# Kernel optimization log

Hardware: AMD Instinct MI355X
Metric: run time of the kernel (lower is better)

## Reference

```python
import jax, jax.numpy as jnp
import numpy as np
from jax import lax

C = 64
KD = 16  # in_channels // k_factor
KS = 3
DN = ('NCHW', 'OIHW', 'NCHW')


def setup_inputs() -> dict:
    key = jax.random.key(0)
    ks = jax.random.split(key, 9)
    B, H, W = 4, 128, 128
    s = 0.05
    return {
        'x': jax.random.normal(ks[0], (B, C, H, W), jnp.float32),
        'y': jax.random.normal(ks[1], (B, C, H, W), jnp.float32),
        'z': jax.random.normal(ks[2], (B, C, H, W), jnp.float32),
        'Wq': jax.random.normal(ks[3], (C, 1, KS, KS), jnp.float32) * s,   # depthwise
        'bq': jax.random.normal(ks[4], (C,), jnp.float32) * s,
        'Wk': jax.random.normal(ks[5], (KD, C, KS, KS), jnp.float32) * s,
        'bk': jax.random.normal(ks[6], (KD,), jnp.float32) * s,
        'wv': jax.random.normal(ks[7], (KD,), jnp.float32) * s,           # 1x1 conv 1->KD
        'bv': jax.random.normal(ks[8], (KD,), jnp.float32) * s,
    }


def reference(x, y, z, Wq, bq, Wk, bk, wv, bv):
    # Q: depthwise 3x3 conv + ReLU on y -> [B,C,H,W]
    q = jax.nn.relu(
        lax.conv_general_dilated(y, Wq, (1, 1), 'SAME',
                                 dimension_numbers=DN, feature_group_count=C)
        + bq[None, :, None, None])
    # K: 3x3 conv C->KD + ReLU on x -> [B,KD,H,W], shared across the C channel axis
    k = jax.nn.relu(
        lax.conv_general_dilated(x, Wk, (1, 1), 'SAME', dimension_numbers=DN)
        + bk[None, :, None, None])
    # V: 1x1 conv 1->KD + ReLU applied per input channel of z -> [B,C,KD,H,W]
    v = jax.nn.relu(z[:, :, None] * wv[None, None, :, None, None]
                    + bv[None, None, :, None, None])
    # Degenerate SDPA: head_dim=1 so scale=1; softmax over the KD 'sequence' axis.
    scores = q[:, :, None] * k[:, None]              # [B,C,KD,H,W]
    attn = jax.nn.softmax(scores, axis=2)
    return jnp.sum(attn * v, axis=2)                 # [B,C,H,W]
```

## Files before the change

### kernel.cpp

```cpp
#include <hip/hip_runtime.h>

#define HH 128
#define WW 128
#define CC 64
#define KD 16
#define HW (HH * WW)
#define HWB (HW * 4)
#define TOTBYTES (4u * CC * HW * 4u)
#define OOB_SENT 0x40000000

typedef __attribute__((ext_vector_type(4))) int   int32x4_t;
typedef __attribute__((ext_vector_type(4))) float floatx4;
typedef __attribute__((ext_vector_type(2))) float floatx2;

__device__ floatx4 llvm_amdgcn_raw_buffer_load_v4f32(int32x4_t srsrc, int voffset,
                                                     int soffset, int aux)
    __asm("llvm.amdgcn.raw.buffer.load.v4f32");
__device__ floatx2 llvm_amdgcn_raw_buffer_load_v2f32(int32x4_t srsrc, int voffset,
                                                     int soffset, int aux)
    __asm("llvm.amdgcn.raw.buffer.load.v2f32");

__device__ inline int32x4_t make_srd(const void* p, unsigned bytes) {
    const unsigned long long a = (unsigned long long)p;
    int32x4_t r;
    r.x = (int)(a & 0xffffffffull);
    r.y = (int)(a >> 32);
    r.z = (int)bytes;
    r.w = 0x00020000;
    return r;
}

#if __has_builtin(__builtin_amdgcn_exp2f)
#define FAST_EXP2(x) __builtin_amdgcn_exp2f(x)
#define KLOG2E 1.44269504088896340736f
#else
#define FAST_EXP2(x) __expf(x)
#define KLOG2E 1.0f
#endif

__global__ __launch_bounds__(512, 1) void repack_wk(const float* __restrict__ Wk,
                                                    float* __restrict__ wsr) {
    const int e = blockIdx.x * 512 + threadIdx.x;
    const int d = e & 15;
    const int r = e >> 4;
    const int t = r % 9;
    const int c = r / 9;
    wsr[e] = Wk[(d * CC + c) * 9 + t];
}

__global__ __launch_bounds__(512, 4) void gatev_fused(
    const float* __restrict__ x, const float* __restrict__ y,
    const float* __restrict__ z,
    const float* __restrict__ wsr,
    const float* __restrict__ Wq, const float* __restrict__ bq,
    const float* __restrict__ bk,
    const float* __restrict__ wv, const float* __restrict__ bv,
    float* __restrict__ out)
{
    __shared__ float lds[16384];

    const int tid  = threadIdx.x;
    const int g    = __builtin_amdgcn_readfirstlane(tid >> 6);
    const int lane = tid & 63;
    const int px16 = lane & 15, py = lane >> 4;
    const int b    = blockIdx.z;
    const int w0   = blockIdx.x * 32 + px16 * 2;
    const int h    = blockIdx.y * 4 + py;
    const int pix  = h * WW + w0;
    const int p0   = py * 32 + px16 * 2;

    const int32x4_t rx = make_srd(x, TOTBYTES);
    const int32x4_t ry = make_srd(y, TOTBYTES);
    const int32x4_t rz = make_srd(z, TOTBYTES);

    const int colb = (w0 > 0 ? w0 - 1 : 0) * 4;
    int rowB[3];
#pragma unroll
    for (int r = 0; r < 3; ++r) {
        const int rr = h - 1 + r;
        rowB[r] = (rr >= 0 && rr < HH) ? rr * WW * 4 + colb : OOB_SENT;
    }
    const bool  intw = (blockIdx.x > 0) & (blockIdx.x < (WW / 32 - 1));
    const float mL = (w0 > 0) ? 1.f : 0.f;
    const float mR = (w0 + 2 < WW) ? 1.f : 0.f;
    const bool  w0e = (w0 == 0);

    const int base = b * CC * HWB;
    const int c0   = __builtin_amdgcn_readfirstlane(g * 8);

    auto mktaps = [&](const floatx4& f, float (&s)[4]) {
        if (intw) { s[0] = f.x; s[1] = f.y; s[2] = f.z; s[3] = f.w; }
        else {
            s[0] = f.x * mL;
            s[1] = w0e ? f.x : f.y;
            s[2] = w0e ? f.y : f.z;
            s[3] = (w0e ? f.z : f.w) * mR;
        }
    };

    floatx2 aP0[8], aP1[8];
#pragma unroll
    for (int i = 0; i < 8; ++i) { aP0[i] = (floatx2){0.f, 0.f}; aP1[i] = (floatx2){0.f, 0.f}; }

    auto load3 = [&](floatx4 (&f)[3], int so) {
#pragma unroll
        for (int r = 0; r < 3; ++r)
            f[r] = llvm_amdgcn_raw_buffer_load_v4f32(rx, rowB[r], so, 0);
    };
    auto compute = [&](const floatx4 (&f)[3], const float* wp) {
        float s[3][4];
#pragma unroll
        for (int r = 0; r < 3; ++r) mktaps(f[r], s[r]);
#pragma unroll
        for (int t = 0; t < 9; ++t) {
            const int tr = t / 3, tc = t % 3;
            const floatx2 t0 = {s[tr][tc],     s[tr][tc]};
            const floatx2 t1 = {s[tr][tc + 1], s[tr][tc + 1]};
#pragma unroll
            for (int j = 0; j < 4; ++j) {
                const floatx4 w4 = *(const floatx4*)&wp[t * 16 + j * 4];
                const floatx2 lo = __builtin_shufflevector(w4, w4, 0, 1);
                const floatx2 hi = __builtin_shufflevector(w4, w4, 2, 3);
                aP0[2 * j + 0] = __builtin_elementwise_fma(lo, t0, aP0[2 * j + 0]);
                aP0[2 * j + 1] = __builtin_elementwise_fma(hi, t0, aP0[2 * j + 1]);
                aP1[2 * j + 0] = __builtin_elementwise_fma(lo, t1, aP1[2 * j + 0]);
                aP1[2 * j + 1] = __builtin_elementwise_fma(hi, t1, aP1[2 * j + 1]);
            }
        }
    };

    {
        floatx4 f0[3], f1[3];
        load3(f0, base + c0 * HWB);
#pragma unroll
        for (int cp = 0; cp < 4; ++cp) {
            load3(f1, base + (c0 + 2 * cp + 1) * HWB);
            compute(f0, wsr + (c0 + 2 * cp) * 144);
            load3(f0, base + (c0 + 2 * cp + 2) * HWB);
            compute(f1, wsr + (c0 + 2 * cp + 1) * 144);
        }
    }

#pragma unroll
    for (int i = 0; i < 8; ++i) {
        *(floatx2*)&lds[g * 2048 + (2 * i + 0) * 128 + p0] = (floatx2){aP0[i].x, aP1[i].x};
        *(floatx2*)&lds[g * 2048 + (2 * i + 1) * 128 + p0] = (floatx2){aP0[i].y, aP1[i].y};
    }
    __syncthreads();

#pragma unroll
    for (int rep = 0; rep < 4; ++rep) {
        const int idx = tid + rep * 512;
        float s = lds[idx];
#pragma unroll
        for (int gg = 1; gg < 8; ++gg) s += lds[gg * 2048 + idx];
        const int d = idx >> 7;
        lds[idx] = fmaxf(s + bk[d], 0.f) * KLOG2E;
    }
    __syncthreads();

    floatx2 kl2[16];
#pragma unroll
    for (int d = 0; d < KD; ++d)
        kl2[d] = *(const floatx2*)&lds[d * 128 + p0];

    auto process = [&](const floatx4 (&f)[3], floatx2 z2, int c) {
        const float* wq = Wq + c * 9;
        float s[3][4];
#pragma unroll
        for (int r = 0; r < 3; ++r) mktaps(f[r], s[r]);
        floatx2 q2 = {bq[c], bq[c]};
#pragma unroll
        for (int t = 0; t < 9; ++t) {
            const int tr = t / 3, tc = t % 3;
            const floatx2 tp2 = {s[tr][tc], s[tr][tc + 1]};
            const floatx2 wq2 = {wq[t], wq[t]};
            q2 = __builtin_elementwise_fma(wq2, tp2, q2);
        }
        const floatx2 zero2 = {0.f, 0.f};
        q2 = __builtin_elementwise_max(q2, zero2);

        floatx2 num2 = zero2, den2 = zero2;
#pragma unroll
        for (int d = 0; d < KD; ++d) {
            const floatx2 s2 = q2 * kl2[d];
            floatx2 e2;
            e2.x = FAST_EXP2(s2.x);
            e2.y = FAST_EXP2(s2.y);
            const floatx2 wv2 = {wv[d], wv[d]};
            const floatx2 bv2 = {bv[d], bv[d]};
            const floatx2 v2 = __builtin_elementwise_max(
                __builtin_elementwise_fma(z2, wv2, bv2), zero2);
            num2 = __builtin_elementwise_fma(e2, v2, num2);
            den2 = den2 + e2;
        }
        floatx2 o2;
        o2.x = __fdividef(num2.x, den2.x);
        o2.y = __fdividef(num2.y, den2.y);
        *(floatx2*)&out[(size_t)b * CC * HW + (size_t)c * HW + pix] = o2;
    };

    auto load3y = [&](floatx4 (&f)[3], floatx2& zz, int so) {
#pragma unroll
        for (int r = 0; r < 3; ++r)
            f[r] = llvm_amdgcn_raw_buffer_load_v4f32(ry, rowB[r], so, 0);
        zz = llvm_amdgcn_raw_buffer_load_v2f32(rz, pix * 4, so, 0);
    };

    {
        floatx4 fy0[3], fy1[3];
        floatx2 z0, z1;
        load3y(fy0, z0, base + c0 * HWB);
#pragma unroll
        for (int cp = 0; cp < 4; ++cp) {
            load3y(fy1, z1, base + (c0 + 2 * cp + 1) * HWB);
            process(fy0, z0, c0 + 2 * cp);
            load3y(fy0, z0, base + (c0 + 2 * cp + 2) * HWB);
            process(fy1, z1, c0 + 2 * cp + 1);
        }
    }
}

extern "C" void kernel_launch(void* const* d_in, const int* in_sizes, int n_in,
                              void* d_out, int out_size, void* d_ws, size_t ws_size,
                              hipStream_t stream) {
    const float* x  = (const float*)d_in[0];
    const float* y  = (const float*)d_in[1];
    const float* z  = (const float*)d_in[2];
    const float* Wq = (const float*)d_in[3];
    const float* bq = (const float*)d_in[4];
    const float* Wk = (const float*)d_in[5];
    const float* bk = (const float*)d_in[6];
    const float* wv = (const float*)d_in[7];
    const float* bv = (const float*)d_in[8];
    float* out = (float*)d_out;
    float* wsr = (float*)d_ws;

    hipLaunchKernelGGL(repack_wk, dim3(18), dim3(512), 0, stream, Wk, wsr);

    dim3 grid(WW / 32, HH / 4, 4);
    dim3 block(512);
    hipLaunchKernelGGL(gatev_fused, grid, block, 0, stream,
                       x, y, z, wsr, Wq, bq, bk, wv, bv, out);
}
```

Baseline: 48.98 us.

## Split fused kernel into separate K-conv and attention kernels via workspace

Result: slower. 50.03 us (+2.2%).

```diff
diff --git a/kernel.cpp b/kernel.cpp
--- a/kernel.cpp
+++ b/kernel.cpp
@@ -46,6 +46,222 @@
     const int t = r % 9;
     const int c = r / 9;
     wsr[e] = Wk[(d * CC + c) * 9 + t];
+}
+
+__global__ __launch_bounds__(512, 8) void kconv(
+    const float* __restrict__ x, const float* __restrict__ wsr,
+    const float* __restrict__ bk, float* __restrict__ kout)
+{
+    __shared__ float lds[8 * KD * 64];
+
+    const int tid  = threadIdx.x;
+    const int g    = __builtin_amdgcn_readfirstlane(tid >> 6);
+    const int lane = tid & 63;
+    const int px   = lane & 15, py = lane >> 4;
+    const int b    = blockIdx.z;
+    const int h    = blockIdx.y * 4 + py;
+    const int w    = blockIdx.x * 16 + px;
+
+    const int32x4_t rx = make_srd(x, TOTBYTES);
+
+    const int colb = (w > 0 ? w - 1 : 0) * 4;
+    int rowB[3];
+#pragma unroll
+    for (int r = 0; r < 3; ++r) {
+        const int rr = h - 1 + r;
+        rowB[r] = (rr >= 0 && rr < HH) ? rr * WW * 4 + colb : OOB_SENT;
+    }
+    const float mL = (w > 0) ? 1.f : 0.f;
+    const float mR = (w < WW - 1) ? 1.f : 0.f;
+    const bool  w0e = (w == 0);
+
+    const int base = b * CC * HWB;
+    const int c0   = __builtin_amdgcn_readfirstlane(g * 8);
+
+    floatx2 a[8];
+#pragma unroll
+    for (int i = 0; i < 8; ++i) a[i] = (floatx2){0.f, 0.f};
+
+    auto load3 = [&](floatx4 (&f)[3], int so) {
+#pragma unroll
+        for (int r = 0; r < 3; ++r)
+            f[r] = llvm_amdgcn_raw_buffer_load_v4f32(rx, rowB[r], so, 0);
+    };
+    auto compute = [&](const floatx4 (&f)[3], const float* wp) {
+        float tp[9];
+#pragma unroll
+        for (int r = 0; r < 3; ++r) {
+            tp[r * 3 + 0] = f[r].x * mL;
+            tp[r * 3 + 1] = w0e ? f[r].x : f[r].y;
+            tp[r * 3 + 2] = (w0e ? f[r].y : f[r].z) * mR;
+        }
+#pragma unroll
+        for (int t = 0; t < 9; ++t) {
+            const floatx2 t2 = {tp[t], tp[t]};
+#pragma unroll
+            for (int j = 0; j < 4; ++j) {
+                const floatx4 w4 = *(const floatx4*)&wp[t * 16 + j * 4];
+                const floatx2 lo = __builtin_shufflevector(w4, w4, 0, 1);
+                const floatx2 hi = __builtin_shufflevector(w4, w4, 2, 3);
+                a[2 * j + 0] = __builtin_elementwise_fma(lo, t2, a[2 * j + 0]);
+                a[2 * j + 1] = __builtin_elementwise_fma(hi, t2, a[2 * j + 1]);
+            }
+        }
+    };
+
+    {
+        floatx4 f0[3], f1[3];
+        load3(f0, base + c0 * HWB);
+#pragma unroll
+        for (int cp = 0; cp < 4; ++cp) {
+            load3(f1, base + (c0 + 2 * cp + 1) * HWB);
+            compute(f0, wsr + (c0 + 2 * cp) * 144);
+            load3(f0, base + (c0 + 2 * cp + 2) * HWB);
+            compute(f1, wsr + (c0 + 2 * cp + 1) * 144);
+        }
+    }
+
+#pragma unroll
+    for (int i = 0; i < 8; ++i) {
+        lds[g * 1024 + (2 * i + 0) * 64 + lane] = a[i].x;
+        lds[g * 1024 + (2 * i + 1) * 64 + lane] = a[i].y;
+    }
+    __syncthreads();
+
+#pragma unroll
+    for (int rep = 0; rep < 2; ++rep) {
+        const int idx = tid + rep * 512;
+        float s = lds[idx];
+#pragma unroll
+        for (int gg = 1; gg < 8; ++gg) s += lds[gg * 1024 + idx];
+        const int d   = idx >> 6;
+        const int pxl = idx & 63;
+        const int hh  = blockIdx.y * 4 + (pxl >> 4);
+        const int ww  = blockIdx.x * 16 + (pxl & 15);
+        kout[(b * KD + d) * HW + hh * WW + ww] =
+            fmaxf(s + bk[d], 0.f) * KLOG2E;
+    }
+}
+
+__global__ __launch_bounds__(512, 4) void attn(
+    const float* __restrict__ y, const float* __restrict__ z,
+    const float* __restrict__ kout,
+    const float* __restrict__ Wq, const float* __restrict__ bq,
+    const float* __restrict__ wv, const float* __restrict__ bv,
+    float* __restrict__ out)
+{
+    __shared__ float klds[KD * 128];
+
+    const int tid  = threadIdx.x;
+    const int g    = __builtin_amdgcn_readfirstlane(tid >> 6);
+    const int lane = tid & 63;
+    const int px16 = lane & 15, py = lane >> 4;
+    const int b    = blockIdx.z;
+    const int w0b  = blockIdx.x * 32;
+    const int h0   = blockIdx.y * 4;
+    const int w0   = w0b + px16 * 2;
+    const int h    = h0 + py;
+    const int pix  = h * WW + w0;
+    const int p0   = py * 32 + px16 * 2;
+
+    const int32x4_t ry = make_srd(y, TOTBYTES);
+    const int32x4_t rz = make_srd(z, TOTBYTES);
+
+#pragma unroll
+    for (int rep = 0; rep < 4; ++rep) {
+        const int idx = tid + rep * 512;
+        const int d   = idx >> 7;
+        const int p   = idx & 127;
+        const int row = p >> 5, col = p & 31;
+        klds[idx] = kout[(b * KD + d) * HW + (h0 + row) * WW + w0b + col];
+    }
+    __syncthreads();
+
+    const int colb = (w0 > 0 ? w0 - 1 : 0) * 4;
+    int rowB[3];
+#pragma unroll
+    for (int r = 0; r < 3; ++r) {
+        const int rr = h - 1 + r;
+        rowB[r] = (rr >= 0 && rr < HH) ? rr * WW * 4 + colb : OOB_SENT;
+    }
+    const bool  intw = (blockIdx.x > 0) & (blockIdx.x < (WW / 32 - 1));
+    const float mL = (w0 > 0) ? 1.f : 0.f;
+    const float mR = (w0 + 2 < WW) ? 1.f : 0.f;
+    const bool  w0e = (w0 == 0);
+
+    const int base = b * CC * HWB;
+    const int c0   = __builtin_amdgcn_readfirstlane(g * 8);
+
+    auto mktaps = [&](const floatx4& f, float (&s)[4]) {
+        if (intw) { s[0] = f.x; s[1] = f.y; s[2] = f.z; s[3] = f.w; }
+        else {
+            s[0] = f.x * mL;
+            s[1] = w0e ? f.x : f.y;
+            s[2] = w0e ? f.y : f.z;
+            s[3] = (w0e ? f.z : f.w) * mR;
+        }
+    };
+
+    floatx2 kl2[16];
+#pragma unroll
+    for (int d = 0; d < KD; ++d)
+        kl2[d] = *(const floatx2*)&klds[d * 128 + p0];
+
+    auto process = [&](const floatx4 (&f)[3], floatx2 z2, int c) {
+        const float* wq = Wq + c * 9;
+        float s[3][4];
+#pragma unroll
+        for (int r = 0; r < 3; ++r) mktaps(f[r], s[r]);
+        floatx2 q2 = {bq[c], bq[c]};
+#pragma unroll
+        for (int t = 0; t < 9; ++t) {
+            const int tr = t / 3, tc = t % 3;
+            const floatx2 tp2 = {s[tr][tc], s[tr][tc + 1]};
+            const floatx2 wq2 = {wq[t], wq[t]};
+            q2 = __builtin_elementwise_fma(wq2, tp2, q2);
+        }
+        const floatx2 zero2 = {0.f, 0.f};
+        q2 = __builtin_elementwise_max(q2, zero2);
+
+        floatx2 num2 = zero2, den2 = zero2;
+#pragma unroll
+        for (int d = 0; d < KD; ++d) {
+            const floatx2 s2 = q2 * kl2[d];
+            floatx2 e2;
+            e2.x = FAST_EXP2(s2.x);
+            e2.y = FAST_EXP2(s2.y);
+            const floatx2 wv2 = {wv[d], wv[d]};
+            const floatx2 bv2 = {bv[d], bv[d]};
+            const floatx2 v2 = __builtin_elementwise_max(
+                __builtin_elementwise_fma(z2, wv2, bv2), zero2);
+            num2 = __builtin_elementwise_fma(e2, v2, num2);
+            den2 = den2 + e2;
+        }
+        floatx2 o2;
+        o2.x = __fdividef(num2.x, den2.x);
+        o2.y = __fdividef(num2.y, den2.y);
+        *(floatx2*)&out[(size_t)b * CC * HW + (size_t)c * HW + pix] = o2;
+    };
+
+    auto load3y = [&](floatx4 (&f)[3], floatx2& zz, int so) {
+#pragma unroll
+        for (int r = 0; r < 3; ++r)
+            f[r] = llvm_amdgcn_raw_buffer_load_v4f32(ry, rowB[r], so, 0);
+        zz = llvm_amdgcn_raw_buffer_load_v2f32(rz, pix * 4, so, 0);
+    };
+
+    {
+        floatx4 fy0[3], fy1[3];
+        floatx2 z0, z1;
+        load3y(fy0, z0, base + c0 * HWB);
+#pragma unroll
+        for (int cp = 0; cp < 4; ++cp) {
+            load3y(fy1, z1, base + (c0 + 2 * cp + 1) * HWB);
+            process(fy0, z0, c0 + 2 * cp);
+            load3y(fy0, z0, base + (c0 + 2 * cp + 2) * HWB);
+            process(fy1, z1, c0 + 2 * cp + 1);
+        }
+    }
 }
 
 __global__ __launch_bounds__(512, 4) void gatev_fused(
@@ -234,12 +450,20 @@
     const float* wv = (const float*)d_in[7];
     const float* bv = (const float*)d_in[8];
     float* out = (float*)d_out;
-    float* wsr = (float*)d_ws;
+
+    float* wsr  = (float*)d_ws;
+    float* kout = (float*)((char*)d_ws + 65536);
+    const size_t need = 65536 + (size_t)4 * KD * HW * 4;
 
     hipLaunchKernelGGL(repack_wk, dim3(18), dim3(512), 0, stream, Wk, wsr);
 
-    dim3 grid(WW / 32, HH / 4, 4);
-    dim3 block(512);
-    hipLaunchKernelGGL(gatev_fused, grid, block, 0, stream,
-                       x, y, z, wsr, Wq, bq, bk, wv, bv, out);
-}
+    if (ws_size >= need) {
+        hipLaunchKernelGGL(kconv, dim3(WW / 16, HH / 4, 4), dim3(512), 0, stream,
+                           x, wsr, bk, kout);
+        hipLaunchKernelGGL(attn, dim3(WW / 32, HH / 4, 4), dim3(512), 0, stream,
+                           y, z, kout, Wq, bq, wv, bv, out);
+    } else {
+        hipLaunchKernelGGL(gatev_fused, dim3(WW / 32, HH / 4, 4), dim3(512), 0, stream,
+                           x, y, z, wsr, Wq, bq, bk, wv, bv, out);
+    }
+}
```
